# Optimization experiments

Hardware: AMD Instinct MI355X
Metric: run time of the kernel (lower is better)

The kernel has to match this reference:

```python
import jax, jax.numpy as jnp
import numpy as np

D_MODEL = 1024
NEG_BIG = -1e9  # matches TF float32 branch


def setup_inputs() -> dict:
    key = jax.random.key(0)
    kq, kk, kv, km = jax.random.split(key, 4)
    B, S, D = 4, 2048, D_MODEL
    q = jax.random.normal(kq, (B, S, D), dtype=jnp.float32)
    k = jax.random.normal(kk, (B, S, D), dtype=jnp.float32)
    v = jax.random.normal(kv, (B, S, D), dtype=jnp.float32)
    mask = jax.random.randint(km, (B, 1, S), 0, 2, dtype=jnp.int32)  # 1 = masked
    return {"q": q, "k": k, "v": v, "mask": mask}


def reference(q, k, v, mask):
    scale = jnp.asarray(D_MODEL, q.dtype) ** -0.5
    # [B,S,S] attention logits
    logits = jnp.einsum("bqd,bkd->bqk", q, k) * scale
    logits = logits + mask.astype(q.dtype) * NEG_BIG
    weights = jax.nn.softmax(logits, axis=-1)
    return jnp.einsum("bqk,bkd->bqd", weights, v)
```

## Files before the change

kernel.cpp:

```cpp
#include <hip/hip_runtime.h>
#include <cstdint>

#define B_    4
#define S_    2048
#define D_    1024
#define SCALE 0.03125f
#define NEG_BIG -1e9f

typedef __attribute__((ext_vector_type(8))) short short8;
typedef __attribute__((ext_vector_type(4))) float f32x4;

__device__ __forceinline__ ushort f2bf(float f) {
  uint32_t u = __float_as_uint(f);
  u += 0x7fffu + ((u >> 16) & 1u);
  return (ushort)(u >> 16);
}

__device__ __forceinline__ void load16_to_lds(const void* g, void* l) {
  __builtin_amdgcn_global_load_lds(
      (const __attribute__((address_space(1))) uint32_t*)g,
      (__attribute__((address_space(3))) uint32_t*)l, 16, 0, 0);
}

#define BAR()   __builtin_amdgcn_s_barrier()
#define LGKM0() do { asm volatile("s_waitcnt lgkmcnt(0)" ::: "memory"); \
                     __builtin_amdgcn_sched_barrier(0); } while (0)
#define VM(n)   asm volatile("s_waitcnt vmcnt(" #n ")" ::: "memory")

__global__ void prep(const float* __restrict__ Q, const float* __restrict__ K,
                     const float* __restrict__ V, ushort* __restrict__ Qb,
                     ushort* __restrict__ Kb, ushort* __restrict__ Vt) {
  __shared__ ushort tile[64][68];
  int id = blockIdx.x;
  if (id < 8192) {
    const float* X = (id < 4096) ? Q : K;
    ushort* Xb     = (id < 4096) ? Qb : Kb;
    int cid = id & 4095;
    size_t i = ((size_t)cid * 256 + threadIdx.x) * 8;
    float4 a = *(const float4*)(X + i);
    float4 c = *(const float4*)(X + i + 4);
    uint4 w;
    w.x = (uint)f2bf(a.x) | ((uint)f2bf(a.y) << 16);
    w.y = (uint)f2bf(a.z) | ((uint)f2bf(a.w) << 16);
    w.z = (uint)f2bf(c.x) | ((uint)f2bf(c.y) << 16);
    w.w = (uint)f2bf(c.z) | ((uint)f2bf(c.w) << 16);
    *(uint4*)(Xb + i) = w;
    return;
  }
  int t = id - 8192;
  int s0 = (t & 31) * 64, d0 = ((t >> 5) & 15) * 64, b = t >> 9;
  int tx = threadIdx.x & 15, ty = threadIdx.x >> 4;
  const float* src = V + ((size_t)b * S_ + s0) * D_ + d0;
  for (int i = 0; i < 4; ++i) {
    int row = ty + i * 16;
    float4 a = *(const float4*)(src + (size_t)row * D_ + tx * 4);
    ushort4 w;
    w.x = f2bf(a.x); w.y = f2bf(a.y); w.z = f2bf(a.z); w.w = f2bf(a.w);
    *(ushort4*)&tile[row][tx * 4] = w;
  }
  __syncthreads();
  ushort* dst = Vt + ((size_t)b * D_ + d0) * S_ + s0;
  for (int i = 0; i < 4; ++i) {
    int drow = ty + i * 16;
    ushort4 w;
    w.x = tile[tx * 4 + 0][drow];
    w.y = tile[tx * 4 + 1][drow];
    w.z = tile[tx * 4 + 2][drow];
    w.w = tile[tx * 4 + 3][drow];
    *(ushort4*)(dst + (size_t)drow * S_ + tx * 4) = w;
  }
}

__global__ __launch_bounds__(512, 2)
void gemm_qk(const ushort* __restrict__ A, const ushort* __restrict__ Bt,
             ushort* __restrict__ C, const int* __restrict__ mask) {
  constexpr int NT  = 1024 / 64;
  constexpr int BUF = 512 * 64;
  constexpr int BO  = 256 * 64;
  __shared__ __align__(16) ushort lds[2 * BUF];

  const int per = gridDim.x >> 3;
  int g  = (blockIdx.x & 7) * per + (blockIdx.x >> 3);
  int b  = g >> 6;
  int t0 = g & 63;
  int bm = t0 >> 3;
  int sn = t0 & 7;
  int bn = (bm & 1) ? 7 - sn : sn;

  int tid = threadIdx.x, lane = tid & 63, wave = tid >> 6;
  int wr = wave >> 2, wc = wave & 3;
  int l16 = lane & 15, quad = lane >> 4;

  const ushort* Ab = A  + (size_t)b * (2048LL * 1024) + (size_t)(bm * 256) * 1024;
  const ushort* Bb = Bt + (size_t)b * (2048LL * 1024) + (size_t)(bn * 256) * 1024;

  float madd[4];
#pragma unroll
  for (int nt = 0; nt < 4; ++nt)
    madd[nt] = mask[b * S_ + bn * 256 + wc * 64 + nt * 16 + l16] ? NEG_BIG : 0.f;

  f32x4 acc[8][4];
#pragma unroll
  for (int i = 0; i < 8; ++i)
#pragma unroll
    for (int j = 0; j < 4; ++j) acc[i][j] = (f32x4){0.f, 0.f, 0.f, 0.f};

  auto stageA = [&](int kt, int half) {
#pragma unroll
    for (int j = 0; j < 2; ++j) {
      int c = tid + j * 512;
      int row = half * 128 + (c >> 3);
      int col = ((c & 7) * 8) ^ ((row & 7) << 3);
      load16_to_lds(Ab + (size_t)row * 1024 + kt * 64 + col,
                    lds + (size_t)(kt & 1) * BUF + (half * 1024 + c) * 8);
    }
  };
  auto stageB = [&](int kt, int half) {
#pragma unroll
    for (int j = 0; j < 2; ++j) {
      int c = tid + j * 512;
      int row = half * 128 + (c >> 3);
      int col = ((c & 7) * 8) ^ ((row & 7) << 3);
      load16_to_lds(Bb + (size_t)row * 1024 + kt * 64 + col,
                    lds + (size_t)(kt & 1) * BUF + BO + (half * 1024 + c) * 8);
    }
  };

  stageA(0, 0); stageA(0, 1); stageB(0, 0); stageB(0, 1);
  stageB(1, 0); stageB(1, 1);
  VM(4);
  BAR();

  for (int t = 0; t < NT; ++t) {
    const ushort* La = lds + (size_t)(t & 1) * BUF;
    const ushort* Lb = La + BO;
    short8 a0[4][2], a1[4][2], b0[2][2], b1[2][2];

    if (t + 1 < NT) stageA(t + 1, 0);
#pragma unroll
    for (int mt = 0; mt < 4; ++mt)
#pragma unroll
      for (int ks = 0; ks < 2; ++ks) {
        int row = wr * 128 + mt * 16 + l16;
        a0[mt][ks] = *(const short8*)(La + row * 64 + ((ks * 32 + quad * 8) ^ ((row & 7) << 3)));
      }
#pragma unroll
    for (int nt = 0; nt < 2; ++nt)
#pragma unroll
      for (int ks = 0; ks < 2; ++ks) {
        int row = wc * 64 + nt * 16 + l16;
        b0[nt][ks] = *(const short8*)(Lb + row * 64 + ((ks * 32 + quad * 8) ^ ((row & 7) << 3)));
      }
    BAR(); LGKM0();
    __builtin_amdgcn_s_setprio(1);
#pragma unroll
    for (int ks = 0; ks < 2; ++ks)
#pragma unroll
      for (int mt = 0; mt < 4; ++mt)
#pragma unroll
        for (int nt = 0; nt < 2; ++nt)
          acc[mt][nt] = __builtin_amdgcn_mfma_f32_16x16x32_bf16(
              a0[mt][ks], b0[nt][ks], acc[mt][nt], 0, 0, 0);
    __builtin_amdgcn_s_setprio(0);
    BAR();

    if (t + 1 < NT) stageA(t + 1, 1);
#pragma unroll
    for (int nt = 0; nt < 2; ++nt)
#pragma unroll
      for (int ks = 0; ks < 2; ++ks) {
        int row = wc * 64 + (nt + 2) * 16 + l16;
        b1[nt][ks] = *(const short8*)(Lb + row * 64 + ((ks * 32 + quad * 8) ^ ((row & 7) << 3)));
      }
#pragma unroll
    for (int mt = 0; mt < 4; ++mt) {
      int row = wr * 128 + (mt + 4) * 16 + l16;
      a1[mt][0] = *(const short8*)(La + row * 64 + ((quad * 8) ^ ((row & 7) << 3)));
    }
    BAR(); LGKM0();
    __builtin_amdgcn_s_setprio(1);
#pragma unroll
    for (int ks = 0; ks < 2; ++ks)
#pragma unroll
      for (int mt = 0; mt < 4; ++mt)
#pragma unroll
        for (int nt = 0; nt < 2; ++nt)
          acc[mt][nt + 2] = __builtin_amdgcn_mfma_f32_16x16x32_bf16(
              a0[mt][ks], b1[nt][ks], acc[mt][nt + 2], 0, 0, 0);
    __builtin_amdgcn_s_setprio(0);
    BAR();

    if (t + 2 < NT) stageB(t + 2, 0);
#pragma unroll
    for (int mt = 0; mt < 4; ++mt) {
      int row = wr * 128 + (mt + 4) * 16 + l16;
      a1[mt][1] = *(const short8*)(La + row * 64 + ((32 + quad * 8) ^ ((row & 7) << 3)));
    }
    BAR(); LGKM0();
    __builtin_amdgcn_s_setprio(1);
#pragma unroll
    for (int ks = 0; ks < 2; ++ks)
#pragma unroll
      for (int mt = 0; mt < 4; ++mt)
#pragma unroll
        for (int nt = 0; nt < 2; ++nt)
          acc[mt + 4][nt + 2] = __builtin_amdgcn_mfma_f32_16x16x32_bf16(
              a1[mt][ks], b1[nt][ks], acc[mt + 4][nt + 2], 0, 0, 0);
    __builtin_amdgcn_s_setprio(0);
    BAR();

    if (t + 2 < NT) stageB(t + 2, 1);
    __builtin_amdgcn_s_setprio(1);
#pragma unroll
    for (int ks = 0; ks < 2; ++ks)
#pragma unroll
      for (int mt = 0; mt < 4; ++mt)
#pragma unroll
        for (int nt = 0; nt < 2; ++nt)
          acc[mt + 4][nt] = __builtin_amdgcn_mfma_f32_16x16x32_bf16(
              a1[mt][ks], b0[nt][ks], acc[mt + 4][nt], 0, 0, 0);
    __builtin_amdgcn_s_setprio(0);

    if (t < NT - 2)      VM(4);
    else if (t == NT - 2) VM(0);
    BAR();
  }

  ushort* Cb = C + (size_t)b * (2048LL * 2048) + (size_t)(bm * 256) * 2048 + bn * 256;
#pragma unroll
  for (int nt = 0; nt < 4; ++nt) {
    int col = wc * 64 + nt * 16 + l16;
#pragma unroll
    for (int mt = 0; mt < 8; ++mt)
#pragma unroll
      for (int r = 0; r < 4; ++r) {
        int row = wr * 128 + mt * 16 + quad * 4 + r;
        Cb[(size_t)row * 2048 + col] = f2bf(acc[mt][nt][r] * SCALE + madd[nt]);
      }
  }
}

__global__ __launch_bounds__(512, 2)
void gemm_pv(const ushort* __restrict__ A, const ushort* __restrict__ Bt,
             float* __restrict__ C) {
  constexpr int NT  = 2048 / 64;
  constexpr int BUF = (256 + 128) * 64;
  constexpr int BO  = 256 * 64;
  __shared__ __align__(16) ushort lds[2 * BUF];

  const int per = gridDim.x >> 3;
  int g  = (blockIdx.x & 7) * per + (blockIdx.x >> 3);
  int b  = g >> 6;
  int t0 = g & 63;
  int bm = t0 >> 3;
  int sn = t0 & 7;
  int bn = (bm & 1) ? 7 - sn : sn;

  int tid = threadIdx.x, lane = tid & 63, wave = tid >> 6;
  int wr = wave >> 1, wc = wave & 1;
  int l16 = lane & 15, quad = lane >> 4;

  const ushort* Ab = A  + (size_t)b * (2048LL * 2048) + (size_t)(bm * 256) * 2048;
  const ushort* Bb = Bt + (size_t)b * (1024LL * 2048) + (size_t)(bn * 128) * 2048;

  f32x4 acc[4][4];
#pragma unroll
  for (int i = 0; i < 4; ++i)
#pragma unroll
    for (int j = 0; j < 4; ++j) acc[i][j] = (f32x4){0.f, 0.f, 0.f, 0.f};

  auto stageA = [&](int kt, int half) {
#pragma unroll
    for (int j = 0; j < 2; ++j) {
      int c = tid + j * 512;
      int row = half * 128 + (c >> 3);
      int col = ((c & 7) * 8) ^ ((row & 7) << 3);
      load16_to_lds(Ab + (size_t)row * 2048 + kt * 64 + col,
                    lds + (size_t)(kt & 1) * BUF + (half * 1024 + c) * 8);
    }
  };
  auto stageB = [&](int kt) {
#pragma unroll
    for (int j = 0; j < 2; ++j) {
      int c = tid + j * 512;
      int row = c >> 3;
      int col = ((c & 7) * 8) ^ ((row & 7) << 3);
      load16_to_lds(Bb + (size_t)row * 2048 + kt * 64 + col,
                    lds + (size_t)(kt & 1) * BUF + BO + c * 8);
    }
  };

  stageA(0, 0); stageA(0, 1); stageB(0);
  stageA(1, 0); stageA(1, 1);
  VM(4);
  BAR();

  for (int t = 0; t < NT; ++t) {
    const ushort* La = lds + (size_t)(t & 1) * BUF;
    const ushort* Lb = La + BO;
    short8 a[4][2], b0[2][2], b1[2][2];

    if (t + 1 < NT) stageB(t + 1);
#pragma unroll
    for (int mt = 0; mt < 4; ++mt)
#pragma unroll
      for (int ks = 0; ks < 2; ++ks) {
        int row = wr * 64 + mt * 16 + l16;
        a[mt][ks] = *(const short8*)(La + row * 64 + ((ks * 32 + quad * 8) ^ ((row & 7) << 3)));
      }
#pragma unroll
    for (int nt = 0; nt < 2; ++nt)
#pragma unroll
      for (int ks = 0; ks < 2; ++ks) {
        int row = wc * 64 + nt * 16 + l16;
        b0[nt][ks] = *(const short8*)(Lb + row * 64 + ((ks * 32 + quad * 8) ^ ((row & 7) << 3)));
      }
    BAR(); LGKM0();
    __builtin_amdgcn_s_setprio(1);
#pragma unroll
    for (int ks = 0; ks < 2; ++ks)
#pragma unroll
      for (int mt = 0; mt < 4; ++mt)
#pragma unroll
        for (int nt = 0; nt < 2; ++nt)
          acc[mt][nt] = __builtin_amdgcn_mfma_f32_16x16x32_bf16(
              a[mt][ks], b0[nt][ks], acc[mt][nt], 0, 0, 0);
    __builtin_amdgcn_s_setprio(0);
    BAR();

    if (t + 2 < NT) { stageA(t + 2, 0); stageA(t + 2, 1); }
#pragma unroll
    for (int nt = 0; nt < 2; ++nt)
#pragma unroll
      for (int ks = 0; ks < 2; ++ks) {
        int row = wc * 64 + (nt + 2) * 16 + l16;
        b1[nt][ks] = *(const short8*)(Lb + row * 64 + ((ks * 32 + quad * 8) ^ ((row & 7) << 3)));
      }
    BAR(); LGKM0();
    __builtin_amdgcn_s_setprio(1);
#pragma unroll
    for (int ks = 0; ks < 2; ++ks)
#pragma unroll
      for (int mt = 0; mt < 4; ++mt)
#pragma unroll
        for (int nt = 0; nt < 2; ++nt)
          acc[mt][nt + 2] = __builtin_amdgcn_mfma_f32_16x16x32_bf16(
              a[mt][ks], b1[nt][ks], acc[mt][nt + 2], 0, 0, 0);
    __builtin_amdgcn_s_setprio(0);

    if (t < NT - 2)      VM(4);
    else if (t == NT - 2) VM(0);
    BAR();
  }

  float* Cb = C + (size_t)b * (2048LL * 1024) + (size_t)(bm * 256) * 1024 + bn * 128;
#pragma unroll
  for (int nt = 0; nt < 4; ++nt) {
    int col = wc * 64 + nt * 16 + l16;
#pragma unroll
    for (int mt = 0; mt < 4; ++mt)
#pragma unroll
      for (int r = 0; r < 4; ++r) {
        int row = wr * 64 + mt * 16 + quad * 4 + r;
        Cb[(size_t)row * 1024 + col] = acc[mt][nt][r];
      }
  }
}

__global__ void softmax_rows(const ushort* __restrict__ S, ushort* __restrict__ P) {
  int row = blockIdx.x * 4 + (threadIdx.x >> 6);
  int lane = threadIdx.x & 63;
  const ushort* src = S + (size_t)row * S_;

  float x[32];
#pragma unroll
  for (int j = 0; j < 4; ++j) {
    uint4 v = *(const uint4*)(src + lane * 8 + j * 512);
    uint32_t w[4] = {v.x, v.y, v.z, v.w};
#pragma unroll
    for (int t = 0; t < 4; ++t) {
      x[j * 8 + t * 2 + 0] = __uint_as_float(w[t] << 16);
      x[j * 8 + t * 2 + 1] = __uint_as_float(w[t] & 0xffff0000u);
    }
  }
  float m = x[0];
#pragma unroll
  for (int i = 1; i < 32; ++i) m = fmaxf(m, x[i]);
  for (int off = 1; off < 64; off <<= 1) m = fmaxf(m, __shfl_xor(m, off));

  float e[32], s = 0.f;
#pragma unroll
  for (int i = 0; i < 32; ++i) { e[i] = __expf(x[i] - m); s += e[i]; }
  for (int off = 1; off < 64; off <<= 1) s += __shfl_xor(s, off);
  float rinv = 1.0f / s;

  ushort* dst = P + (size_t)row * S_;
#pragma unroll
  for (int j = 0; j < 4; ++j) {
    uint4 w;
    uint32_t* pw = &w.x;
#pragma unroll
    for (int t = 0; t < 4; ++t)
      pw[t] = (uint32_t)f2bf(e[j * 8 + t * 2] * rinv) |
              ((uint32_t)f2bf(e[j * 8 + t * 2 + 1] * rinv) << 16);
    *(uint4*)(dst + lane * 8 + j * 512) = w;
  }
}

extern "C" void kernel_launch(void* const* d_in, const int* in_sizes, int n_in,
                              void* d_out, int out_size, void* d_ws, size_t ws_size,
                              hipStream_t stream) {
  const float* Q   = (const float*)d_in[0];
  const float* K   = (const float*)d_in[1];
  const float* V   = (const float*)d_in[2];
  const int*  mask = (const int*)d_in[3];
  float* Out = (float*)d_out;

  const size_t E = (size_t)B_ * S_ * D_;
  ushort* Qb = (ushort*)d_ws;
  ushort* Kb = Qb + E;
  ushort* Vt = Kb + E;
  ushort* Sb = Vt + E;
  ushort* P  = Qb;

  prep<<<10240, 256, 0, stream>>>(Q, K, V, Qb, Kb, Vt);

  gemm_qk<<<256, 512, 0, stream>>>(Qb, Kb, Sb, mask);

  softmax_rows<<<2048, 256, 0, stream>>>(Sb, P);

  gemm_pv<<<256, 512, 0, stream>>>(P, Vt, Out);
}
```

Baseline: 225.7 us.

## Restructure GEMM prefetch pipelines into full-tile double buffering with fewer barriers

Both the QK and PV GEMM kernels now issue all global-to-LDS loads for tile t+2 after the current buffer's fragments are read into registers. Loads for tile t+1 are fully staged before the loop starts. This removes several intra-iteration barriers and LDS waits, at the cost of holding more fragment registers and more outstanding loads. The softmax scale is also folded into the Q bf16 conversion in prep, which drops a multiply from the QK epilogue, and the prep conversion is rewritten as two coalesced 4-wide halves.

```diff
diff --git a/kernel.cpp b/kernel.cpp
--- a/kernel.cpp
+++ b/kernel.cpp
@@ -30,21 +30,21 @@
 __global__ void prep(const float* __restrict__ Q, const float* __restrict__ K,
                      const float* __restrict__ V, ushort* __restrict__ Qb,
                      ushort* __restrict__ Kb, ushort* __restrict__ Vt) {
-  __shared__ ushort tile[64][68];
+  __shared__ ushort tile[64][66];
   int id = blockIdx.x;
   if (id < 8192) {
     const float* X = (id < 4096) ? Q : K;
     ushort* Xb     = (id < 4096) ? Qb : Kb;
-    int cid = id & 4095;
-    size_t i = ((size_t)cid * 256 + threadIdx.x) * 8;
-    float4 a = *(const float4*)(X + i);
-    float4 c = *(const float4*)(X + i + 4);
-    uint4 w;
-    w.x = (uint)f2bf(a.x) | ((uint)f2bf(a.y) << 16);
-    w.y = (uint)f2bf(a.z) | ((uint)f2bf(a.w) << 16);
-    w.z = (uint)f2bf(c.x) | ((uint)f2bf(c.y) << 16);
-    w.w = (uint)f2bf(c.z) | ((uint)f2bf(c.w) << 16);
-    *(uint4*)(Xb + i) = w;
+    float s        = (id < 4096) ? SCALE : 1.0f;
+    size_t base = (size_t)(id & 4095) * 2048 + threadIdx.x * 4;
+#pragma unroll
+    for (int h = 0; h < 2; ++h) {
+      float4 a = *(const float4*)(X + base + h * 1024);
+      uint2 w;
+      w.x = (uint)f2bf(a.x * s) | ((uint)f2bf(a.y * s) << 16);
+      w.y = (uint)f2bf(a.z * s) | ((uint)f2bf(a.w * s) << 16);
+      *(uint2*)(Xb + base + h * 1024) = w;
+    }
     return;
   }
   int t = id - 8192;
@@ -126,9 +126,9 @@
     }
   };
 
-  stageA(0, 0); stageA(0, 1); stageB(0, 0); stageB(0, 1);
-  stageB(1, 0); stageB(1, 1);
-  VM(4);
+  stageA(0, 0); stageB(0, 0); stageA(0, 1); stageB(0, 1);
+  stageA(1, 0); stageB(1, 0); stageA(1, 1); stageB(1, 1);
+  VM(8);
   BAR();
 
   for (int t = 0; t < NT; ++t) {
@@ -136,7 +136,6 @@
     const ushort* Lb = La + BO;
     short8 a0[4][2], a1[4][2], b0[2][2], b1[2][2];
 
-    if (t + 1 < NT) stageA(t + 1, 0);
 #pragma unroll
     for (int mt = 0; mt < 4; ++mt)
 #pragma unroll
@@ -164,7 +163,13 @@
     __builtin_amdgcn_s_setprio(0);
     BAR();
 
-    if (t + 1 < NT) stageA(t + 1, 1);
+#pragma unroll
+    for (int mt = 0; mt < 4; ++mt)
+#pragma unroll
+      for (int ks = 0; ks < 2; ++ks) {
+        int row = wr * 128 + (mt + 4) * 16 + l16;
+        a1[mt][ks] = *(const short8*)(La + row * 64 + ((ks * 32 + quad * 8) ^ ((row & 7) << 3)));
+      }
 #pragma unroll
     for (int nt = 0; nt < 2; ++nt)
 #pragma unroll
@@ -172,11 +177,6 @@
         int row = wc * 64 + (nt + 2) * 16 + l16;
         b1[nt][ks] = *(const short8*)(Lb + row * 64 + ((ks * 32 + quad * 8) ^ ((row & 7) << 3)));
       }
-#pragma unroll
-    for (int mt = 0; mt < 4; ++mt) {
-      int row = wr * 128 + (mt + 4) * 16 + l16;
-      a1[mt][0] = *(const short8*)(La + row * 64 + ((quad * 8) ^ ((row & 7) << 3)));
-    }
     BAR(); LGKM0();
     __builtin_amdgcn_s_setprio(1);
 #pragma unroll
@@ -190,13 +190,7 @@
     __builtin_amdgcn_s_setprio(0);
     BAR();
 
-    if (t + 2 < NT) stageB(t + 2, 0);
-#pragma unroll
-    for (int mt = 0; mt < 4; ++mt) {
-      int row = wr * 128 + (mt + 4) * 16 + l16;
-      a1[mt][1] = *(const short8*)(La + row * 64 + ((32 + quad * 8) ^ ((row & 7) << 3)));
-    }
-    BAR(); LGKM0();
+    if (t + 2 < NT) { stageA(t + 2, 0); stageB(t + 2, 0); }
     __builtin_amdgcn_s_setprio(1);
 #pragma unroll
     for (int ks = 0; ks < 2; ++ks)
@@ -207,9 +201,8 @@
           acc[mt + 4][nt + 2] = __builtin_amdgcn_mfma_f32_16x16x32_bf16(
               a1[mt][ks], b1[nt][ks], acc[mt + 4][nt + 2], 0, 0, 0);
     __builtin_amdgcn_s_setprio(0);
-    BAR();
-
-    if (t + 2 < NT) stageB(t + 2, 1);
+
+    if (t + 2 < NT) { stageA(t + 2, 1); stageB(t + 2, 1); }
     __builtin_amdgcn_s_setprio(1);
 #pragma unroll
     for (int ks = 0; ks < 2; ++ks)
@@ -221,9 +214,8 @@
               a1[mt][ks], b0[nt][ks], acc[mt + 4][nt], 0, 0, 0);
     __builtin_amdgcn_s_setprio(0);
 
-    if (t < NT - 2)      VM(4);
-    else if (t == NT - 2) VM(0);
-    BAR();
+    if (t < NT - 2)       { VM(8); BAR(); }
+    else if (t == NT - 2) { VM(0); BAR(); }
   }
 
   ushort* Cb = C + (size_t)b * (2048LL * 2048) + (size_t)(bm * 256) * 2048 + bn * 256;
@@ -235,7 +227,7 @@
 #pragma unroll
       for (int r = 0; r < 4; ++r) {
         int row = wr * 128 + mt * 16 + quad * 4 + r;
-        Cb[(size_t)row * 2048 + col] = f2bf(acc[mt][nt][r] * SCALE + madd[nt]);
+        Cb[(size_t)row * 2048 + col] = f2bf(acc[mt][nt][r] + madd[nt]);
       }
   }
 }
@@ -291,8 +283,8 @@
   };
 
   stageA(0, 0); stageA(0, 1); stageB(0);
-  stageA(1, 0); stageA(1, 1);
-  VM(4);
+  stageA(1, 0); stageA(1, 1); stageB(1);
+  VM(6);
   BAR();
 
   for (int t = 0; t < NT; ++t) {
@@ -300,7 +292,6 @@
     const ushort* Lb = La + BO;
     short8 a[4][2], b0[2][2], b1[2][2];
 
-    if (t + 1 < NT) stageB(t + 1);
 #pragma unroll
     for (int mt = 0; mt < 4; ++mt)
 #pragma unroll
@@ -314,6 +305,8 @@
       for (int ks = 0; ks < 2; ++ks) {
         int row = wc * 64 + nt * 16 + l16;
         b0[nt][ks] = *(const short8*)(Lb + row * 64 + ((ks * 32 + quad * 8) ^ ((row & 7) << 3)));
+        int row2 = wc * 64 + (nt + 2) * 16 + l16;
+        b1[nt][ks] = *(const short8*)(Lb + row2 * 64 + ((ks * 32 + quad * 8) ^ ((row2 & 7) << 3)));
       }
     BAR(); LGKM0();
     __builtin_amdgcn_s_setprio(1);
@@ -328,15 +321,7 @@
     __builtin_amdgcn_s_setprio(0);
     BAR();
 
-    if (t + 2 < NT) { stageA(t + 2, 0); stageA(t + 2, 1); }
-#pragma unroll
-    for (int nt = 0; nt < 2; ++nt)
-#pragma unroll
-      for (int ks = 0; ks < 2; ++ks) {
-        int row = wc * 64 + (nt + 2) * 16 + l16;
-        b1[nt][ks] = *(const short8*)(Lb + row * 64 + ((ks * 32 + quad * 8) ^ ((row & 7) << 3)));
-      }
-    BAR(); LGKM0();
+    if (t + 2 < NT) { stageA(t + 2, 0); stageA(t + 2, 1); stageB(t + 2); }
     __builtin_amdgcn_s_setprio(1);
 #pragma unroll
     for (int ks = 0; ks < 2; ++ks)
@@ -348,9 +333,8 @@
               a[mt][ks], b1[nt][ks], acc[mt][nt + 2], 0, 0, 0);
     __builtin_amdgcn_s_setprio(0);
 
-    if (t < NT - 2)      VM(4);
-    else if (t == NT - 2) VM(0);
-    BAR();
+    if (t < NT - 2)       { VM(6); BAR(); }
+    else if (t == NT - 2) { VM(0); BAR(); }
   }
 
   float* Cb = C + (size_t)b * (2048LL * 1024) + (size_t)(bm * 256) * 1024 + bn * 128;
```

New measurement: 227.5 us. Within noise of the previous version (+0.8%).
